# Kernel tuning notes

Measured on AMD Instinct MI355X. Metric: run time of the kernel, lower is better.

The kernel has to match this reference:

```python
import jax, jax.numpy as jnp
import numpy as np

B, L, C, K, S = 8, 4096, 512, 5, 8


def setup_inputs() -> dict:
    key = jax.random.key(0)
    ks = jax.random.split(key, 5)
    x = jax.random.normal(ks[0], (B, L, C), dtype=jnp.float32)
    # contiguous random partition of [0, L) into S segments per batch row
    rng = np.random.default_rng(0)
    cuts = np.sort(rng.integers(1, L, size=(B, S - 1)), axis=1)
    starts = np.concatenate([np.zeros((B, 1), np.int64), cuts.astype(np.int64)], axis=1)
    ends = np.concatenate([cuts.astype(np.int64), np.full((B, 1), L, np.int64)], axis=1)
    segment_boundaries = jnp.asarray(np.stack([starts, ends], axis=-1))  # [B,S,2]
    fan = 1.0 / np.sqrt(K)
    w_dw = jax.random.normal(ks[1], (C, K), dtype=jnp.float32) * fan
    b_dw = jax.random.normal(ks[2], (C,), dtype=jnp.float32) * 0.01
    w_pw = jax.random.normal(ks[3], (C, C), dtype=jnp.float32) * (1.0 / np.sqrt(C))
    b_pw = jax.random.normal(ks[4], (C,), dtype=jnp.float32) * 0.01
    return {"x": x, "segment_boundaries": segment_boundaries,
            "w_dw": w_dw, "b_dw": b_dw, "w_pw": w_pw, "b_pw": b_pw}


def reference(x, segment_boundaries, w_dw, b_dw, w_pw, b_pw):
    # x: [B,L,C]; segment_boundaries: [B,S,2]; w_dw: [C,K]; w_pw: [C_out,C_in]
    Bx, Lx, Cx = x.shape
    Kx = w_dw.shape[1]
    starts = segment_boundaries[..., 0]  # [B,S]
    ends = segment_boundaries[..., 1]    # [B,S]
    pos = jnp.arange(Lx)
    in_seg = (pos[None, None, :] >= starts[..., None]) & (pos[None, None, :] < ends[..., None])  # [B,S,L]
    covered = in_seg.any(axis=1)                                  # [B,L]
    seg_id = jnp.where(covered, jnp.argmax(in_seg, axis=1), -1)   # [B,L]

    # causal depthwise conv with left zero-pad per segment (no cross-segment leakage)
    acc = jnp.zeros_like(x)
    for d in range(Kx):  # d = how far back we look; tap index = K-1-d
        if d == 0:
            x_s, id_s = x, seg_id
        else:
            x_s = jnp.pad(x, ((0, 0), (d, 0), (0, 0)))[:, :Lx]
            id_s = jnp.pad(seg_id, ((0, 0), (d, 0)), constant_values=-2)[:, :Lx]
        m = ((seg_id == id_s) & covered).astype(x.dtype)          # [B,L]
        acc = acc + w_dw[:, Kx - 1 - d] * x_s * m[..., None]
    dw = acc + b_dw                                               # [B,L,C]
    pw = jnp.einsum('blc,dc->bld', dw, w_pw) + b_pw               # pointwise 1x1 conv
    return pw * covered[..., None].astype(x.dtype)                # zeros outside segments
```

## Files before the change

### kernel.cpp

```cpp
#include <hip/hip_runtime.h>
#include <hip/hip_bf16.h>
#include <climits>

typedef __bf16 bf16;
typedef __bf16 bf16x4 __attribute__((ext_vector_type(4)));
typedef __bf16 bf16x8 __attribute__((ext_vector_type(8)));
typedef float f32x4 __attribute__((ext_vector_type(4)));

#define NB 8
#define L_ 4096
#define C_ 512
#define KW 5
#define NS 8
#define BM 64

__global__ __launch_bounds__(256) void prep_kernel(
    const float* __restrict__ w_pw, const float* __restrict__ b_dw,
    const float* __restrict__ b_pw, bf16* __restrict__ pk,
    float* __restrict__ bias2) {
  const int t = threadIdx.x;
  if (blockIdx.x < 128) {
    const int gid = blockIdx.x * 256 + t;
    const int lane = gid & 63;
    const int nf = (gid >> 6) & 3;
    const int wnn = (gid >> 8) & 7;
    const int kk = gid >> 11;
    const int n = wnn * 64 + nf * 16 + (lane & 15);
    const int c = kk * 32 + (lane >> 4) * 8;
    const float* s = w_pw + n * C_ + c;
    float4 a = *(const float4*)s;
    float4 b4 = *(const float4*)(s + 4);
    bf16x8 h;
    h[0] = (bf16)a.x; h[1] = (bf16)a.y; h[2] = (bf16)a.z; h[3] = (bf16)a.w;
    h[4] = (bf16)b4.x; h[5] = (bf16)b4.y; h[6] = (bf16)b4.z; h[7] = (bf16)b4.w;
    *(bf16x8*)(pk + (size_t)gid * 8) = h;
  } else {
    const int n = blockIdx.x - 128;
    float2 v = *(const float2*)(w_pw + n * C_ + 2 * t);
    float2 bb = *(const float2*)(b_dw + 2 * t);
    float s = v.x * bb.x + v.y * bb.y;
#pragma unroll
    for (int off = 32; off; off >>= 1) s += __shfl_down(s, off, 64);
    __shared__ float part[4];
    if ((t & 63) == 0) part[t >> 6] = s;
    __syncthreads();
    if (t == 0) bias2[n] = b_pw[n] + part[0] + part[1] + part[2] + part[3];
  }
}

__global__ __launch_bounds__(512, 4) void fused_kernel(
    const float* __restrict__ x, const int* __restrict__ segb,
    const float* __restrict__ w_dw, const bf16* __restrict__ pk,
    const float* __restrict__ bias2, float* __restrict__ out) {
  __shared__ __align__(16) bf16 As[BM * C_];

  const int t = threadIdx.x;
  const int lane = t & 63;
  const int b = blockIdx.x >> 6;
  const int l0 = (blockIdx.x & 63) << 6;

  const int q = t & 127;
  const int r0 = (t >> 7) << 4;

  float4 raw[5];
#pragma unroll
  for (int i = 0; i < 5; ++i)
    raw[i] = *(const float4*)(w_dw + q * 20 + i * 4);
  f32x4 wt[5];
#pragma unroll
  for (int m = 0; m < 5; ++m)
#pragma unroll
    for (int i = 0; i < 4; ++i) {
      const int f = i * 5 + m;
      wt[m][i] = ((const float*)&raw[f >> 2])[f & 3];
    }

  const int* sb = segb + b * NS * 2;
  int stv[NS];
#pragma unroll
  for (int s = 0; s < NS; ++s) stv[s] = sb[2 * s];
  auto nxt = [&](int l) {
    int nn = INT_MAX;
#pragma unroll
    for (int s = 0; s < NS; ++s)
      nn = (stv[s] > l && stv[s] < nn) ? stv[s] : nn;
    return nn;
  };
  int ns = nxt(l0 + r0 - 4);

  const float* gxb = x + (size_t)(b * L_ + l0 + r0) * C_ + q * 4;

  const f32x4 z4 = (f32x4){0.f, 0.f, 0.f, 0.f};
  f32x4 w0 = z4, w1 = z4, w2 = z4, w3 = z4;

  f32x4 p0[4], p1[4], p2[4];
  auto ldg = [&](int g, f32x4 (&p)[4]) {
#pragma unroll
    for (int j = 0; j < 4; ++j)
      p[j] = *(const f32x4*)(gxb + (ptrdiff_t)(g * 4 + j) * C_);
  };
  ldg(0, p0);
  ldg(1, p1);
  ldg(2, p2);

#pragma unroll
  for (int i = 0; i < 4; ++i) {
    const int l = l0 + r0 - 4 + i;
    f32x4 nv = z4;
    if (l >= 0) nv = *(const f32x4*)(gxb + (ptrdiff_t)(i - 4) * C_);
    if (l == ns) { w0 = z4; w1 = z4; w2 = z4; w3 = z4; ns = nxt(l); }
    w0 = w1; w1 = w2; w2 = w3; w3 = nv;
  }

  auto dorow = [&](int l, f32x4& A, f32x4& B4, f32x4& Cc, f32x4& D,
                   const f32x4& E, int rloc) {
    if (l == ns) { A = z4; B4 = z4; Cc = z4; D = z4; ns = nxt(l); }
    f32x4 r;
#pragma unroll
    for (int i = 0; i < 4; ++i) {
      float a = A[i] * wt[0][i];
      a = fmaf(B4[i], wt[1][i], a);
      a = fmaf(Cc[i], wt[2][i], a);
      a = fmaf(D[i], wt[3][i], a);
      a = fmaf(E[i], wt[4][i], a);
      r[i] = a;
    }
    bf16x4 h;
#pragma unroll
    for (int i = 0; i < 4; ++i) h[i] = (bf16)r[i];
    const int u = q ^ ((rloc & 7) << 1);
    *(bf16x4*)&As[rloc * 512 + u * 4] = h;
  };

  auto compute = [&](int g, f32x4 (&p)[4]) {
    const int lb = l0 + r0 + g * 4;
    dorow(lb + 0, w0, w1, w2, w3, p[0], r0 + g * 4 + 0);
    dorow(lb + 1, w1, w2, w3, p[0], p[1], r0 + g * 4 + 1);
    dorow(lb + 2, w2, w3, p[0], p[1], p[2], r0 + g * 4 + 2);
    dorow(lb + 3, w3, p[0], p[1], p[2], p[3], r0 + g * 4 + 3);
    w0 = p[0]; w1 = p[1]; w2 = p[2]; w3 = p[3];
  };

  compute(0, p0);
  ldg(3, p0);
  compute(1, p1);
  compute(2, p2);
  compute(3, p0);

  __syncthreads();

  const int wn = t >> 6;
  const int cg = lane >> 4;
  const int rx = lane & 7;

  int aRow[4];
#pragma unroll
  for (int mf = 0; mf < 4; ++mf) aRow[mf] = (mf * 16 + (lane & 15)) * 512;
  const bf16* pw = pk + (size_t)wn * 2048 + lane * 8;

  f32x4 acc[4][4];
#pragma unroll
  for (int i = 0; i < 4; ++i)
#pragma unroll
    for (int j = 0; j < 4; ++j) acc[i][j] = z4;

#pragma unroll 1
  for (int kk = 0; kk < 16; ++kk) {
    const bf16* pws = pw + kk * 16384;
    bf16x8 bb[4];
#pragma unroll
    for (int nf = 0; nf < 4; ++nf)
      bb[nf] = *(const bf16x8*)(pws + nf * 512);
    const int ao = ((kk * 4 + cg) ^ rx) << 3;
    bf16x8 af[4];
#pragma unroll
    for (int mf = 0; mf < 4; ++mf)
      af[mf] = *(const bf16x8*)&As[aRow[mf] + ao];
    __builtin_amdgcn_s_setprio(1);
#pragma unroll
    for (int nf = 0; nf < 4; ++nf)
#pragma unroll
      for (int mf = 0; mf < 4; ++mf)
        acc[mf][nf] = __builtin_amdgcn_mfma_f32_16x16x32_bf16(
            af[mf], bb[nf], acc[mf][nf], 0, 0, 0);
    __builtin_amdgcn_s_setprio(0);
  }

  const int col0 = wn * 64 + (lane & 15);
  float bia[4];
#pragma unroll
  for (int nf = 0; nf < 4; ++nf) bia[nf] = bias2[col0 + nf * 16];
  const int rb0 = l0 + (cg << 2);
#pragma unroll
  for (int mf = 0; mf < 4; ++mf) {
#pragma unroll
    for (int i = 0; i < 4; ++i) {
      const int row = rb0 + mf * 16 + i;
      float* o = out + (size_t)(b * L_ + row) * C_ + col0;
#pragma unroll
      for (int nf = 0; nf < 4; ++nf) o[nf * 16] = acc[mf][nf][i] + bia[nf];
    }
  }
}

extern "C" void kernel_launch(void* const* d_in, const int* in_sizes, int n_in,
                              void* d_out, int out_size, void* d_ws,
                              size_t ws_size, hipStream_t stream) {
  const float* x = (const float*)d_in[0];
  const int* segb = (const int*)d_in[1];
  const float* w_dw = (const float*)d_in[2];
  const float* b_dw = (const float*)d_in[3];
  const float* w_pw = (const float*)d_in[4];
  const float* b_pw = (const float*)d_in[5];
  float* out = (float*)d_out;

  float* bias2 = (float*)d_ws;
  bf16* pk = (bf16*)((char*)d_ws + 4096);

  prep_kernel<<<640, 256, 0, stream>>>(w_pw, b_dw, b_pw, pk, bias2);
  fused_kernel<<<NB * L_ / BM, 512, 0, stream>>>(x, segb, w_dw, pk, bias2,
                                                 out);
}
```

Measured before the change: 39.93 us.

## Warp-specialize fused kernel to overlap depthwise conv of second half with GEMM of first

All warps first compute the depthwise conv for the first 32 rows. Then warps 0-3 run the pointwise GEMM on those rows with a 2x8 MFMA tile per warp, while warps 4-7 compute the depthwise conv for rows 32-63 and then run the GEMM on them. The aim is to overlap global loads and VALU work with MFMA work inside one block. Launch bounds drop to 2 blocks per SM to leave room for the larger accumulator tiles. The risks are load imbalance between the warp groups, lower occupancy, and hand-placed barriers whose counts must match across both branches.

Result: slower. 42.91 us (+7.4%).

```diff
diff --git a/kernel.cpp b/kernel.cpp
--- a/kernel.cpp
+++ b/kernel.cpp
@@ -13,6 +13,18 @@
 #define KW 5
 #define NS 8
 #define BM 64
+
+#define BARRIER_MEM                                                            \
+  do {                                                                         \
+    __builtin_amdgcn_sched_barrier(0);                                         \
+    __builtin_amdgcn_s_barrier();                                              \
+    __builtin_amdgcn_sched_barrier(0);                                         \
+  } while (0)
+#define DSFLUSH_BARRIER                                                        \
+  do {                                                                         \
+    asm volatile("s_waitcnt lgkmcnt(0)" ::: "memory");                         \
+    BARRIER_MEM;                                                               \
+  } while (0)
 
 __global__ __launch_bounds__(256) void prep_kernel(
     const float* __restrict__ w_pw, const float* __restrict__ b_dw,
@@ -23,9 +35,9 @@
     const int gid = blockIdx.x * 256 + t;
     const int lane = gid & 63;
     const int nf = (gid >> 6) & 3;
-    const int wnn = (gid >> 8) & 7;
+    const int g = (gid >> 8) & 7;
     const int kk = gid >> 11;
-    const int n = wnn * 64 + nf * 16 + (lane & 15);
+    const int n = g * 64 + nf * 16 + (lane & 15);
     const int c = kk * 32 + (lane >> 4) * 8;
     const float* s = w_pw + n * C_ + c;
     float4 a = *(const float4*)s;
@@ -48,7 +60,7 @@
   }
 }
 
-__global__ __launch_bounds__(512, 4) void fused_kernel(
+__global__ __launch_bounds__(512, 2) void fused_kernel(
     const float* __restrict__ x, const int* __restrict__ segb,
     const float* __restrict__ w_dw, const bf16* __restrict__ pk,
     const float* __restrict__ bias2, float* __restrict__ out) {
@@ -56,11 +68,12 @@
 
   const int t = threadIdx.x;
   const int lane = t & 63;
+  const int wid = t >> 6;
   const int b = blockIdx.x >> 6;
   const int l0 = (blockIdx.x & 63) << 6;
 
+  const f32x4 z4 = (f32x4){0.f, 0.f, 0.f, 0.f};
   const int q = t & 127;
-  const int r0 = (t >> 7) << 4;
 
   float4 raw[5];
 #pragma unroll
@@ -74,7 +87,6 @@
       const int f = i * 5 + m;
       wt[m][i] = ((const float*)&raw[f >> 2])[f & 3];
     }
-
   const int* sb = segb + b * NS * 2;
   int stv[NS];
 #pragma unroll
@@ -86,31 +98,9 @@
       nn = (stv[s] > l && stv[s] < nn) ? stv[s] : nn;
     return nn;
   };
-  int ns = nxt(l0 + r0 - 4);
-
-  const float* gxb = x + (size_t)(b * L_ + l0 + r0) * C_ + q * 4;
-
-  const f32x4 z4 = (f32x4){0.f, 0.f, 0.f, 0.f};
+
   f32x4 w0 = z4, w1 = z4, w2 = z4, w3 = z4;
-
-  f32x4 p0[4], p1[4], p2[4];
-  auto ldg = [&](int g, f32x4 (&p)[4]) {
-#pragma unroll
-    for (int j = 0; j < 4; ++j)
-      p[j] = *(const f32x4*)(gxb + (ptrdiff_t)(g * 4 + j) * C_);
-  };
-  ldg(0, p0);
-  ldg(1, p1);
-  ldg(2, p2);
-
-#pragma unroll
-  for (int i = 0; i < 4; ++i) {
-    const int l = l0 + r0 - 4 + i;
-    f32x4 nv = z4;
-    if (l >= 0) nv = *(const f32x4*)(gxb + (ptrdiff_t)(i - 4) * C_);
-    if (l == ns) { w0 = z4; w1 = z4; w2 = z4; w3 = z4; ns = nxt(l); }
-    w0 = w1; w1 = w2; w2 = w3; w3 = nv;
-  }
+  int ns = 0;
 
   auto dorow = [&](int l, f32x4& A, f32x4& B4, f32x4& Cc, f32x4& D,
                    const f32x4& E, int rloc) {
@@ -132,74 +122,137 @@
     *(bf16x4*)&As[rloc * 512 + u * 4] = h;
   };
 
-  auto compute = [&](int g, f32x4 (&p)[4]) {
-    const int lb = l0 + r0 + g * 4;
-    dorow(lb + 0, w0, w1, w2, w3, p[0], r0 + g * 4 + 0);
-    dorow(lb + 1, w1, w2, w3, p[0], p[1], r0 + g * 4 + 1);
-    dorow(lb + 2, w2, w3, p[0], p[1], p[2], r0 + g * 4 + 2);
-    dorow(lb + 3, w3, p[0], p[1], p[2], p[3], r0 + g * 4 + 3);
-    w0 = p[0]; w1 = p[1]; w2 = p[2]; w3 = p[3];
-  };
-
-  compute(0, p0);
-  ldg(3, p0);
-  compute(1, p1);
-  compute(2, p2);
-  compute(3, p0);
-
-  __syncthreads();
-
-  const int wn = t >> 6;
+  {
+    const int r0 = (t >> 7) << 3;
+    ns = nxt(l0 + r0 - 4);
+    const float* gxb = x + (size_t)(b * L_ + l0 + r0) * C_ + q * 4;
+    f32x4 hw[4], p0[4], p1[4];
+#pragma unroll
+    for (int i = 0; i < 4; ++i) {
+      const int lw = l0 + r0 - 4 + i;
+      hw[i] = (lw >= 0) ? *(const f32x4*)(gxb + (ptrdiff_t)(i - 4) * C_) : z4;
+    }
+#pragma unroll
+    for (int j = 0; j < 4; ++j)
+      p0[j] = *(const f32x4*)(gxb + (ptrdiff_t)j * C_);
+#pragma unroll
+    for (int j = 0; j < 4; ++j)
+      p1[j] = *(const f32x4*)(gxb + (ptrdiff_t)(4 + j) * C_);
+#pragma unroll
+    for (int i = 0; i < 4; ++i) {
+      const int l = l0 + r0 - 4 + i;
+      if (l == ns) { w0 = z4; w1 = z4; w2 = z4; w3 = z4; ns = nxt(l); }
+      w0 = w1; w1 = w2; w2 = w3; w3 = hw[i];
+    }
+    const int lb = l0 + r0;
+    dorow(lb + 0, w0, w1, w2, w3, p0[0], r0 + 0);
+    dorow(lb + 1, w1, w2, w3, p0[0], p0[1], r0 + 1);
+    dorow(lb + 2, w2, w3, p0[0], p0[1], p0[2], r0 + 2);
+    dorow(lb + 3, w3, p0[0], p0[1], p0[2], p0[3], r0 + 3);
+    w0 = p0[0]; w1 = p0[1]; w2 = p0[2]; w3 = p0[3];
+    dorow(lb + 4, w0, w1, w2, w3, p1[0], r0 + 4);
+    dorow(lb + 5, w1, w2, w3, p1[0], p1[1], r0 + 5);
+    dorow(lb + 6, w2, w3, p1[0], p1[1], p1[2], r0 + 6);
+    dorow(lb + 7, w3, p1[0], p1[1], p1[2], p1[3], r0 + 7);
+  }
+
   const int cg = lane >> 4;
   const int rx = lane & 7;
-
-  int aRow[4];
-#pragma unroll
-  for (int mf = 0; mf < 4; ++mf) aRow[mf] = (mf * 16 + (lane & 15)) * 512;
-  const bf16* pw = pk + (size_t)wn * 2048 + lane * 8;
-
-  f32x4 acc[4][4];
-#pragma unroll
-  for (int i = 0; i < 4; ++i)
-#pragma unroll
-    for (int j = 0; j < 4; ++j) acc[i][j] = z4;
-
+  f32x4 acc[2][8];
+#pragma unroll
+  for (int i = 0; i < 2; ++i)
+#pragma unroll
+    for (int j = 0; j < 8; ++j) acc[i][j] = z4;
+
+  auto gemm_half = [&](int rowOff, int wn) {
+    const int aRow0 = (rowOff + (lane & 15)) * 512;
+    const int aRow1 = aRow0 + 16 * 512;
+    const bf16* pb = pk + (size_t)wn * 4096 + lane * 8;
 #pragma unroll 1
-  for (int kk = 0; kk < 16; ++kk) {
-    const bf16* pws = pw + kk * 16384;
-    bf16x8 bb[4];
-#pragma unroll
-    for (int nf = 0; nf < 4; ++nf)
-      bb[nf] = *(const bf16x8*)(pws + nf * 512);
-    const int ao = ((kk * 4 + cg) ^ rx) << 3;
-    bf16x8 af[4];
-#pragma unroll
-    for (int mf = 0; mf < 4; ++mf)
-      af[mf] = *(const bf16x8*)&As[aRow[mf] + ao];
-    __builtin_amdgcn_s_setprio(1);
-#pragma unroll
-    for (int nf = 0; nf < 4; ++nf)
-#pragma unroll
-      for (int mf = 0; mf < 4; ++mf)
-        acc[mf][nf] = __builtin_amdgcn_mfma_f32_16x16x32_bf16(
-            af[mf], bb[nf], acc[mf][nf], 0, 0, 0);
-    __builtin_amdgcn_s_setprio(0);
-  }
-
-  const int col0 = wn * 64 + (lane & 15);
-  float bia[4];
-#pragma unroll
-  for (int nf = 0; nf < 4; ++nf) bia[nf] = bias2[col0 + nf * 16];
-  const int rb0 = l0 + (cg << 2);
-#pragma unroll
-  for (int mf = 0; mf < 4; ++mf) {
-#pragma unroll
-    for (int i = 0; i < 4; ++i) {
-      const int row = rb0 + mf * 16 + i;
-      float* o = out + (size_t)(b * L_ + row) * C_ + col0;
-#pragma unroll
-      for (int nf = 0; nf < 4; ++nf) o[nf * 16] = acc[mf][nf][i] + bia[nf];
-    }
+    for (int kk = 0; kk < 16; ++kk) {
+      const bf16* pws = pb + kk * 16384;
+      bf16x8 bb[8];
+#pragma unroll
+      for (int nf = 0; nf < 8; ++nf)
+        bb[nf] = *(const bf16x8*)(pws + nf * 512);
+      const int ao = ((kk * 4 + cg) ^ rx) << 3;
+      bf16x8 a0 = *(const bf16x8*)&As[aRow0 + ao];
+      bf16x8 a1 = *(const bf16x8*)&As[aRow1 + ao];
+      __builtin_amdgcn_s_setprio(1);
+#pragma unroll
+      for (int nf = 0; nf < 8; ++nf) {
+        acc[0][nf] = __builtin_amdgcn_mfma_f32_16x16x32_bf16(a0, bb[nf],
+                                                             acc[0][nf], 0, 0, 0);
+        acc[1][nf] = __builtin_amdgcn_mfma_f32_16x16x32_bf16(a1, bb[nf],
+                                                             acc[1][nf], 0, 0, 0);
+      }
+      __builtin_amdgcn_s_setprio(0);
+    }
+  };
+
+  auto epilogue = [&](int rowOff, int wn) {
+    const int col0 = wn * 128 + (lane & 15);
+    float bia[8];
+#pragma unroll
+    for (int nf = 0; nf < 8; ++nf) bia[nf] = bias2[col0 + nf * 16];
+    const int rb0 = l0 + rowOff + (cg << 2);
+#pragma unroll
+    for (int mf = 0; mf < 2; ++mf) {
+#pragma unroll
+      for (int i = 0; i < 4; ++i) {
+        const int row = rb0 + mf * 16 + i;
+        float* o = out + (size_t)(b * L_ + row) * C_ + col0;
+#pragma unroll
+        for (int nf = 0; nf < 8; ++nf) o[nf * 16] = acc[mf][nf][i] + bia[nf];
+      }
+    }
+  };
+
+  DSFLUSH_BARRIER;
+
+  if (wid < 4) {
+    gemm_half(0, wid);
+    BARRIER_MEM;
+    epilogue(0, wid);
+  } else {
+    const int r0 = 32 + (((t >> 7) - 2) << 4);
+    ns = nxt(l0 + r0 - 4);
+    const float* gxb = x + (size_t)(b * L_ + l0 + r0) * C_ + q * 4;
+    f32x4 p0[4], p1[4], p2[4];
+    auto ldg = [&](int g, f32x4 (&p)[4]) {
+#pragma unroll
+      for (int j = 0; j < 4; ++j)
+        p[j] = *(const f32x4*)(gxb + (ptrdiff_t)(g * 4 + j) * C_);
+    };
+    ldg(0, p0);
+    ldg(1, p1);
+    ldg(2, p2);
+    w0 = z4; w1 = z4; w2 = z4; w3 = z4;
+#pragma unroll
+    for (int i = 0; i < 4; ++i) {
+      const int l = l0 + r0 - 4 + i;
+      f32x4 nv = *(const f32x4*)(gxb + (ptrdiff_t)(i - 4) * C_);
+      if (l == ns) { w0 = z4; w1 = z4; w2 = z4; w3 = z4; ns = nxt(l); }
+      w0 = w1; w1 = w2; w2 = w3; w3 = nv;
+    }
+    auto compute = [&](int g, f32x4 (&p)[4]) {
+      const int lb = l0 + r0 + g * 4;
+      const int rl = r0 + g * 4;
+      dorow(lb + 0, w0, w1, w2, w3, p[0], rl + 0);
+      dorow(lb + 1, w1, w2, w3, p[0], p[1], rl + 1);
+      dorow(lb + 2, w2, w3, p[0], p[1], p[2], rl + 2);
+      dorow(lb + 3, w3, p[0], p[1], p[2], p[3], rl + 3);
+      w0 = p[0]; w1 = p[1]; w2 = p[2]; w3 = p[3];
+    };
+    compute(0, p0);
+    ldg(3, p0);
+    compute(1, p1);
+    compute(2, p2);
+    compute(3, p0);
+
+    DSFLUSH_BARRIER;
+    gemm_half(32, wid - 4);
+    epilogue(32, wid - 4);
   }
 }
 
```

## Process two row tiles per block, overlapping second conv with first GEMM

Applied to the files above, without the earlier changes.

Each block now handles 128 rows as two 64-row tiles with double-buffered LDS. The depthwise conv for the second tile is interleaved with the MFMA GEMM steps of the first tile, so global loads and VALU work overlap the matrix work. The cost is half as many blocks, twice the LDS per block and a lower occupancy hint, which may reduce latency hiding across waves.

New measurement: 43.25 us. 1.08x slower.

```diff
diff --git a/kernel.cpp b/kernel.cpp
--- a/kernel.cpp
+++ b/kernel.cpp
@@ -13,6 +13,18 @@
 #define KW 5
 #define NS 8
 #define BM 64
+
+#define BARRIER_MEM                                                            \
+  do {                                                                         \
+    __builtin_amdgcn_sched_barrier(0);                                         \
+    __builtin_amdgcn_s_barrier();                                              \
+    __builtin_amdgcn_sched_barrier(0);                                         \
+  } while (0)
+#define DSFLUSH_BARRIER                                                        \
+  do {                                                                         \
+    asm volatile("s_waitcnt lgkmcnt(0)" ::: "memory");                         \
+    BARRIER_MEM;                                                               \
+  } while (0)
 
 __global__ __launch_bounds__(256) void prep_kernel(
     const float* __restrict__ w_pw, const float* __restrict__ b_dw,
@@ -48,17 +60,18 @@
   }
 }
 
-__global__ __launch_bounds__(512, 4) void fused_kernel(
+__global__ __launch_bounds__(512, 2) void fused_kernel(
     const float* __restrict__ x, const int* __restrict__ segb,
     const float* __restrict__ w_dw, const bf16* __restrict__ pk,
     const float* __restrict__ bias2, float* __restrict__ out) {
-  __shared__ __align__(16) bf16 As[BM * C_];
+  __shared__ __align__(16) bf16 As[2][BM * C_];
 
   const int t = threadIdx.x;
   const int lane = t & 63;
-  const int b = blockIdx.x >> 6;
-  const int l0 = (blockIdx.x & 63) << 6;
-
+  const int b = blockIdx.x >> 5;
+  const int l0 = (blockIdx.x & 31) << 7;
+
+  const f32x4 z4 = (f32x4){0.f, 0.f, 0.f, 0.f};
   const int q = t & 127;
   const int r0 = (t >> 7) << 4;
 
@@ -74,7 +87,6 @@
       const int f = i * 5 + m;
       wt[m][i] = ((const float*)&raw[f >> 2])[f & 3];
     }
-
   const int* sb = segb + b * NS * 2;
   int stv[NS];
 #pragma unroll
@@ -86,33 +98,11 @@
       nn = (stv[s] > l && stv[s] < nn) ? stv[s] : nn;
     return nn;
   };
-  int ns = nxt(l0 + r0 - 4);
-
-  const float* gxb = x + (size_t)(b * L_ + l0 + r0) * C_ + q * 4;
-
-  const f32x4 z4 = (f32x4){0.f, 0.f, 0.f, 0.f};
+
   f32x4 w0 = z4, w1 = z4, w2 = z4, w3 = z4;
-
-  f32x4 p0[4], p1[4], p2[4];
-  auto ldg = [&](int g, f32x4 (&p)[4]) {
-#pragma unroll
-    for (int j = 0; j < 4; ++j)
-      p[j] = *(const f32x4*)(gxb + (ptrdiff_t)(g * 4 + j) * C_);
-  };
-  ldg(0, p0);
-  ldg(1, p1);
-  ldg(2, p2);
-
-#pragma unroll
-  for (int i = 0; i < 4; ++i) {
-    const int l = l0 + r0 - 4 + i;
-    f32x4 nv = z4;
-    if (l >= 0) nv = *(const f32x4*)(gxb + (ptrdiff_t)(i - 4) * C_);
-    if (l == ns) { w0 = z4; w1 = z4; w2 = z4; w3 = z4; ns = nxt(l); }
-    w0 = w1; w1 = w2; w2 = w3; w3 = nv;
-  }
-
-  auto dorow = [&](int l, f32x4& A, f32x4& B4, f32x4& Cc, f32x4& D,
+  int ns = 0;
+
+  auto dorow = [&](bf16* dst, int l, f32x4& A, f32x4& B4, f32x4& Cc, f32x4& D,
                    const f32x4& E, int rloc) {
     if (l == ns) { A = z4; B4 = z4; Cc = z4; D = z4; ns = nxt(l); }
     f32x4 r;
@@ -129,30 +119,49 @@
 #pragma unroll
     for (int i = 0; i < 4; ++i) h[i] = (bf16)r[i];
     const int u = q ^ ((rloc & 7) << 1);
-    *(bf16x4*)&As[rloc * 512 + u * 4] = h;
-  };
-
-  auto compute = [&](int g, f32x4 (&p)[4]) {
-    const int lb = l0 + r0 + g * 4;
-    dorow(lb + 0, w0, w1, w2, w3, p[0], r0 + g * 4 + 0);
-    dorow(lb + 1, w1, w2, w3, p[0], p[1], r0 + g * 4 + 1);
-    dorow(lb + 2, w2, w3, p[0], p[1], p[2], r0 + g * 4 + 2);
-    dorow(lb + 3, w3, p[0], p[1], p[2], p[3], r0 + g * 4 + 3);
-    w0 = p[0]; w1 = p[1]; w2 = p[2]; w3 = p[3];
-  };
-
-  compute(0, p0);
-  ldg(3, p0);
-  compute(1, p1);
-  compute(2, p2);
-  compute(3, p0);
-
-  __syncthreads();
+    *(bf16x4*)&dst[rloc * 512 + u * 4] = h;
+  };
+
+  {
+    ns = nxt(l0 + r0 - 4);
+    const float* gxb = x + (size_t)(b * L_ + l0 + r0) * C_ + q * 4;
+    f32x4 p0[4], p1[4], p2[4];
+    auto ldg = [&](int g, f32x4 (&p)[4]) {
+#pragma unroll
+      for (int j = 0; j < 4; ++j)
+        p[j] = *(const f32x4*)(gxb + (ptrdiff_t)(g * 4 + j) * C_);
+    };
+    ldg(0, p0);
+    ldg(1, p1);
+    ldg(2, p2);
+#pragma unroll
+    for (int i = 0; i < 4; ++i) {
+      const int l = l0 + r0 - 4 + i;
+      f32x4 nv = z4;
+      if (l >= 0) nv = *(const f32x4*)(gxb + (ptrdiff_t)(i - 4) * C_);
+      if (l == ns) { w0 = z4; w1 = z4; w2 = z4; w3 = z4; ns = nxt(l); }
+      w0 = w1; w1 = w2; w2 = w3; w3 = nv;
+    }
+    auto compute = [&](int g, f32x4 (&p)[4]) {
+      const int lb = l0 + r0 + g * 4;
+      const int rl = r0 + g * 4;
+      dorow((bf16*)As[0], lb + 0, w0, w1, w2, w3, p[0], rl + 0);
+      dorow((bf16*)As[0], lb + 1, w1, w2, w3, p[0], p[1], rl + 1);
+      dorow((bf16*)As[0], lb + 2, w2, w3, p[0], p[1], p[2], rl + 2);
+      dorow((bf16*)As[0], lb + 3, w3, p[0], p[1], p[2], p[3], rl + 3);
+      w0 = p[0]; w1 = p[1]; w2 = p[2]; w3 = p[3];
+    };
+    compute(0, p0);
+    ldg(3, p0);
+    compute(1, p1);
+    compute(2, p2);
+    compute(3, p0);
+  }
+  DSFLUSH_BARRIER;
 
   const int wn = t >> 6;
   const int cg = lane >> 4;
   const int rx = lane & 7;
-
   int aRow[4];
 #pragma unroll
   for (int mf = 0; mf < 4; ++mf) aRow[mf] = (mf * 16 + (lane & 15)) * 512;
@@ -164,8 +173,7 @@
 #pragma unroll
     for (int j = 0; j < 4; ++j) acc[i][j] = z4;
 
-#pragma unroll 1
-  for (int kk = 0; kk < 16; ++kk) {
+  auto gemm_step = [&](const bf16* Ab, int kk) {
     const bf16* pws = pw + kk * 16384;
     bf16x8 bb[4];
 #pragma unroll
@@ -175,7 +183,7 @@
     bf16x8 af[4];
 #pragma unroll
     for (int mf = 0; mf < 4; ++mf)
-      af[mf] = *(const bf16x8*)&As[aRow[mf] + ao];
+      af[mf] = *(const bf16x8*)&Ab[aRow[mf] + ao];
     __builtin_amdgcn_s_setprio(1);
 #pragma unroll
     for (int nf = 0; nf < 4; ++nf)
@@ -184,23 +192,86 @@
         acc[mf][nf] = __builtin_amdgcn_mfma_f32_16x16x32_bf16(
             af[mf], bb[nf], acc[mf][nf], 0, 0, 0);
     __builtin_amdgcn_s_setprio(0);
-  }
-
-  const int col0 = wn * 64 + (lane & 15);
-  float bia[4];
-#pragma unroll
-  for (int nf = 0; nf < 4; ++nf) bia[nf] = bias2[col0 + nf * 16];
-  const int rb0 = l0 + (cg << 2);
-#pragma unroll
-  for (int mf = 0; mf < 4; ++mf) {
-#pragma unroll
-    for (int i = 0; i < 4; ++i) {
-      const int row = rb0 + mf * 16 + i;
-      float* o = out + (size_t)(b * L_ + row) * C_ + col0;
-#pragma unroll
-      for (int nf = 0; nf < 4; ++nf) o[nf * 16] = acc[mf][nf][i] + bia[nf];
-    }
-  }
+  };
+
+  auto epilogue = [&](int tileOff) {
+    const int col0 = wn * 64 + (lane & 15);
+    float bia[4];
+#pragma unroll
+    for (int nf = 0; nf < 4; ++nf) bia[nf] = bias2[col0 + nf * 16];
+    const int rb0 = l0 + tileOff + (cg << 2);
+#pragma unroll
+    for (int mf = 0; mf < 4; ++mf) {
+#pragma unroll
+      for (int i = 0; i < 4; ++i) {
+        const int row = rb0 + mf * 16 + i;
+        float* o = out + (size_t)(b * L_ + row) * C_ + col0;
+#pragma unroll
+        for (int nf = 0; nf < 4; ++nf) o[nf * 16] = acc[mf][nf][i] + bia[nf];
+      }
+    }
+  };
+
+  {
+    ns = nxt(l0 + 64 + r0 - 4);
+    const float* gxb1 = x + (size_t)(b * L_ + l0 + 64 + r0) * C_ + q * 4;
+    f32x4 pA[4], pB[4];
+    auto ldg1 = [&](int g, f32x4 (&p)[4]) {
+#pragma unroll
+      for (int j = 0; j < 4; ++j)
+        p[j] = *(const f32x4*)(gxb1 + (ptrdiff_t)(g * 4 + j) * C_);
+    };
+    {
+      f32x4 hw[4];
+#pragma unroll
+      for (int i = 0; i < 4; ++i)
+        hw[i] = *(const f32x4*)(gxb1 + (ptrdiff_t)(i - 4) * C_);
+      ldg1(0, pA);
+      w0 = z4; w1 = z4; w2 = z4; w3 = z4;
+#pragma unroll
+      for (int i = 0; i < 4; ++i) {
+        const int l = l0 + 64 + r0 - 4 + i;
+        if (l == ns) { w0 = z4; w1 = z4; w2 = z4; w3 = z4; ns = nxt(l); }
+        w0 = w1; w1 = w2; w2 = w3; w3 = hw[i];
+      }
+    }
+    auto convg = [&](int g, f32x4 (&p)[4]) {
+      const int lb = l0 + 64 + r0 + g * 4;
+      const int rl = r0 + g * 4;
+      dorow((bf16*)As[1], lb + 0, w0, w1, w2, w3, p[0], rl + 0);
+      dorow((bf16*)As[1], lb + 1, w1, w2, w3, p[0], p[1], rl + 1);
+      dorow((bf16*)As[1], lb + 2, w2, w3, p[0], p[1], p[2], rl + 2);
+      dorow((bf16*)As[1], lb + 3, w3, p[0], p[1], p[2], p[3], rl + 3);
+      w0 = p[0]; w1 = p[1]; w2 = p[2]; w3 = p[3];
+    };
+    const bf16* A0 = (const bf16*)As[0];
+    ldg1(1, pB);
+    convg(0, pA);
+    gemm_step(A0, 0); gemm_step(A0, 1); gemm_step(A0, 2); gemm_step(A0, 3);
+    ldg1(2, pA);
+    convg(1, pB);
+    gemm_step(A0, 4); gemm_step(A0, 5); gemm_step(A0, 6); gemm_step(A0, 7);
+    ldg1(3, pB);
+    convg(2, pA);
+    gemm_step(A0, 8); gemm_step(A0, 9); gemm_step(A0, 10); gemm_step(A0, 11);
+    convg(3, pB);
+    gemm_step(A0, 12); gemm_step(A0, 13); gemm_step(A0, 14); gemm_step(A0, 15);
+  }
+
+  epilogue(0);
+
+  DSFLUSH_BARRIER;
+
+#pragma unroll
+  for (int i = 0; i < 4; ++i)
+#pragma unroll
+    for (int j = 0; j < 4; ++j) acc[i][j] = z4;
+  {
+    const bf16* A1 = (const bf16*)As[1];
+#pragma unroll 1
+    for (int kk = 0; kk < 16; ++kk) gemm_step(A1, kk);
+  }
+  epilogue(64);
 }
 
 extern "C" void kernel_launch(void* const* d_in, const int* in_sizes, int n_in,
@@ -218,6 +289,6 @@
   bf16* pk = (bf16*)((char*)d_ws + 4096);
 
   prep_kernel<<<640, 256, 0, stream>>>(w_pw, b_dw, b_pw, pk, bias2);
-  fused_kernel<<<NB * L_ / BM, 512, 0, stream>>>(x, segb, w_dw, pk, bias2,
-                                                 out);
+  fused_kernel<<<NB * L_ / 128, 512, 0, stream>>>(x, segb, w_dw, pk, bias2,
+                                                  out);
 }
```
